# Kernel tuning notes

Measured on AMD Instinct MI355X. Metric: run time of the kernel, lower is better.

The kernel has to match this reference:

```python
import jax, jax.numpy as jnp
import numpy as np

D_MODEL = 1024
HEADS = 16
D_K = D_MODEL // HEADS  # 64
LN_EPS = 1e-5


def setup_inputs() -> dict:
    key = jax.random.key(0)
    ks = jax.random.split(key, 9)
    B, S = 4, 2048
    x = jax.random.normal(ks[0], (B, S, D_MODEL), dtype=jnp.float32)
    s = 1.0 / np.sqrt(D_K)
    # Per-head linear weights, stacked over heads: [H, d_in, d_out]
    Wq = jax.random.uniform(ks[1], (HEADS, D_K, D_K), jnp.float32, -s, s)
    Wk = jax.random.uniform(ks[2], (HEADS, D_K, D_K), jnp.float32, -s, s)
    Wv = jax.random.uniform(ks[3], (HEADS, D_K, D_K), jnp.float32, -s, s)
    bq = jax.random.uniform(ks[4], (HEADS, D_K), jnp.float32, -s, s)
    bk = jax.random.uniform(ks[5], (HEADS, D_K), jnp.float32, -s, s)
    bv = jax.random.uniform(ks[6], (HEADS, D_K), jnp.float32, -s, s)
    gamma = jnp.ones((D_MODEL,), jnp.float32)
    beta = jnp.zeros((D_MODEL,), jnp.float32)
    return {"x": x, "Wq": Wq, "Wk": Wk, "Wv": Wv,
            "bq": bq, "bk": bk, "bv": bv, "gamma": gamma, "beta": beta}


def reference(x, Wq, Wk, Wv, bq, bk, bv, gamma, beta):
    B, S, D = x.shape
    scale = jnp.sqrt(jnp.asarray(D_K, x.dtype))
    # chunk(x, heads, -1) == reshape to [B,S,H,d_k]
    xh = x.reshape(B, S, HEADS, D_K)
    # Batched per-head linears (replaces the Python loop over heads)
    Q = jnp.einsum('bshd,hde->bshe', xh, Wq) + bq  # [B,S,H,d_k]
    K = jnp.einsum('bshd,hde->bshe', xh, Wk) + bk
    V = jnp.einsum('bshd,hde->bshe', xh, Wv) + bv
    scores = jnp.einsum('bshd,bthd->bhst', Q, K) / scale  # [B,H,S,S]
    A = jax.nn.softmax(scores, axis=-1)
    out = jnp.einsum('bhst,bthd->bshd', A, V).reshape(B, S, D)
    # dropout is identity in eval mode; residual + LayerNorm
    y = out + x
    mu = jnp.mean(y, axis=-1, keepdims=True)
    var = jnp.mean((y - mu) ** 2, axis=-1, keepdims=True)
    return (y - mu) * jax.lax.rsqrt(var + LN_EPS) * gamma + beta
```

## Files before the change

kernel.cpp:

```cpp
#include <hip/hip_runtime.h>
#include <math.h>

typedef __bf16 bf16_t;
typedef __bf16 bf16x8 __attribute__((ext_vector_type(8)));
typedef __bf16 bf16x4 __attribute__((ext_vector_type(4)));
typedef short short4v __attribute__((ext_vector_type(4)));
typedef float f32x4 __attribute__((ext_vector_type(4)));

#define LOG2E 1.4426950408889634f

#if __has_builtin(__builtin_amdgcn_exp2f)
#define FAST_EXP2(x) __builtin_amdgcn_exp2f(x)
#else
#define FAST_EXP2(x) exp2f(x)
#endif

constexpr int BATCH = 4;
constexpr int SEQ = 2048;
constexpr int NHEADS = 16;
constexpr int DK = 64;
constexpr int DMODEL = 1024;
constexpr int NTOK = BATCH * SEQ;

constexpr size_t WT_OFF   = 0;
constexpr size_t BIAS_OFF = WT_OFF + (size_t)3*16*64*64*2;
constexpr size_t Q_OFF    = BIAS_OFF + (size_t)3*16*64*4;
constexpr size_t QSZ      = (size_t)BATCH*NHEADS*SEQ*DK*2;
constexpr size_t K_OFF    = Q_OFF + QSZ;
constexpr size_t VT_OFF   = K_OFF + QSZ;
constexpr size_t O_OFF    = VT_OFF + QSZ;

__global__ __launch_bounds__(256) void prep_kernel(
    const float* __restrict__ Wq, const float* __restrict__ Wk,
    const float* __restrict__ Wv, const float* __restrict__ bq,
    const float* __restrict__ bk, const float* __restrict__ bv,
    bf16_t* __restrict__ Wt, float* __restrict__ bias)
{
    const float QS = 0.125f * LOG2E;
    int i = blockIdx.x * 256 + threadIdx.x;
    if (i < 3*16*64*64) {
        int d = i & 63, e = (i >> 6) & 63, h = (i >> 12) & 15, p = i >> 16;
        const float* W = (p == 0) ? Wq : (p == 1) ? Wk : Wv;
        float v = W[(h*64 + d)*64 + e] * ((p == 0) ? QS : 1.0f);
        Wt[i] = (bf16_t)v;
    }
    if (i < 3*16*64) {
        int e = i & 63, h = (i >> 6) & 15, p = i >> 10;
        const float* bb = (p == 0) ? bq : (p == 1) ? bk : bv;
        bias[i] = bb[h*64 + e] * ((p == 0) ? QS : 1.0f);
    }
}

__global__ __launch_bounds__(256) void qkv_kernel(
    const float* __restrict__ x, const bf16_t* __restrict__ Wt,
    const float* __restrict__ bias,
    bf16_t* __restrict__ Q, bf16_t* __restrict__ Kg, bf16_t* __restrict__ Vt)
{
    constexpr int QSTR = 72;
    __shared__ bf16_t Slds[4][16 * QSTR];
    const int tid = threadIdx.x;
    const int w = tid >> 6, lane = tid & 63;
    const int ln = lane & 15, quad = lane >> 4;
    const int gw = blockIdx.x * 4 + w;
    const int h = gw & 15, tt = gw >> 4;
    const int t0 = tt * 16;
    const int b = t0 >> 11;
    const int s0 = t0 & 2047;
    const int bh = b * 16 + h;

    bf16x8 afrag[2];
#pragma unroll
    for (int kc = 0; kc < 2; kc++) {
        const float* xp = &x[(size_t)(t0 + ln)*DMODEL + h*DK + kc*32 + quad*8];
        float4 u0 = *(const float4*)xp;
        float4 u1 = *(const float4*)(xp + 4);
        bf16x8 a;
        a[0]=(bf16_t)u0.x; a[1]=(bf16_t)u0.y; a[2]=(bf16_t)u0.z; a[3]=(bf16_t)u0.w;
        a[4]=(bf16_t)u1.x; a[5]=(bf16_t)u1.y; a[6]=(bf16_t)u1.z; a[7]=(bf16_t)u1.w;
        afrag[kc] = a;
    }

#pragma unroll
    for (int p = 0; p < 3; p++) {
#pragma unroll
        for (int nt = 0; nt < 4; nt++) {
            const bf16_t* wp = &Wt[((size_t)((p*16 + h)*64) + nt*16 + ln)*64 + quad*8];
            bf16x8 b0 = *(const bf16x8*)wp;
            bf16x8 b1 = *(const bf16x8*)(wp + 32);
            f32x4 acc = {0.f, 0.f, 0.f, 0.f};
            acc = __builtin_amdgcn_mfma_f32_16x16x32_bf16(afrag[0], b0, acc, 0, 0, 0);
            acc = __builtin_amdgcn_mfma_f32_16x16x32_bf16(afrag[1], b1, acc, 0, 0, 0);
            float bv = bias[(p*16 + h)*64 + nt*16 + ln];
#pragma unroll
            for (int r = 0; r < 4; r++)
                Slds[w][(quad*4 + r)*QSTR + nt*16 + ln] = (bf16_t)(acc[r] + bv);
        }
        if (p < 2) {
            bf16_t* dst = (p == 0) ? Q : Kg;
            const int row = lane >> 2, c = (lane & 3) * 16;
            bf16_t* dp = &dst[((size_t)bh*SEQ + s0 + row)*DK + c];
            *(uint4*)dp       = *(const uint4*)&Slds[w][row*QSTR + c];
            *(uint4*)(dp + 8) = *(const uint4*)&Slds[w][row*QSTR + c + 8];
        } else {
            unsigned int packed[8];
#pragma unroll
            for (int i = 0; i < 8; i++) {
                unsigned short lo = __builtin_bit_cast(unsigned short, Slds[w][(2*i  )*QSTR + lane]);
                unsigned short hi = __builtin_bit_cast(unsigned short, Slds[w][(2*i+1)*QSTR + lane]);
                packed[i] = (unsigned)lo | ((unsigned)hi << 16);
            }
            bf16_t* vp = &Vt[((size_t)bh*DK + lane)*SEQ + s0];
            uint4 v0; v0.x = packed[0]; v0.y = packed[1]; v0.z = packed[2]; v0.w = packed[3];
            uint4 v1; v1.x = packed[4]; v1.y = packed[5]; v1.z = packed[6]; v1.w = packed[7];
            *(uint4*)(vp)     = v0;
            *(uint4*)(vp + 8) = v1;
        }
    }
}

__global__ __launch_bounds__(256, 2) void flash_kernel(
    const bf16_t* __restrict__ Q, const bf16_t* __restrict__ Kg,
    const bf16_t* __restrict__ Vt, bf16_t* __restrict__ O)
{
    constexpr int LSTR = 72;
    __shared__ union {
        struct { bf16_t K[64 * LSTR]; bf16_t V[64 * LSTR]; } kv;
        bf16_t O[4][32 * LSTR];
    } sh;

    const int tid = threadIdx.x;
    const int w = tid >> 6, lane = tid & 63;
    const int ln = lane & 15, quad = lane >> 4;
    const int bh = blockIdx.x >> 4;
    const int qt = blockIdx.x & 15;
    const int q0 = qt * 128 + w * 32;

    bf16x8 qfrag[2][2];
#pragma unroll
    for (int st = 0; st < 2; st++)
#pragma unroll
        for (int kc = 0; kc < 2; kc++)
            qfrag[st][kc] = *(const bf16x8*)
                &Q[((size_t)bh*SEQ + q0 + st*16 + ln)*DK + kc*32 + quad*8];

    f32x4 o[2][4];
#pragma unroll
    for (int st = 0; st < 2; st++)
#pragma unroll
        for (int dt = 0; dt < 4; dt++)
            o[st][dt] = (f32x4){0.f, 0.f, 0.f, 0.f};
    float l_[2] = {0.f, 0.f};

    const bf16_t* kbase = &Kg[(size_t)bh * SEQ * DK];
    const bf16_t* vbase = &Vt[(size_t)bh * DK * SEQ];

    const int srow = tid >> 3, scol = (tid & 7) * 8;

    for (int ci = 0; ci < SEQ / 64; ci++) {
        __syncthreads();
        {
            uint4 k0 = *(const uint4*)&kbase[((size_t)(ci*64 + srow))*DK + scol];
            uint4 k1 = *(const uint4*)&kbase[((size_t)(ci*64 + srow + 32))*DK + scol];
            uint4 v0 = *(const uint4*)&vbase[(size_t)srow*SEQ + ci*64 + scol];
            uint4 v1 = *(const uint4*)&vbase[(size_t)(srow + 32)*SEQ + ci*64 + scol];
            *(uint4*)&sh.kv.K[srow*LSTR + scol]        = k0;
            *(uint4*)&sh.kv.K[(srow + 32)*LSTR + scol] = k1;
            *(uint4*)&sh.kv.V[srow*LSTR + scol]        = v0;
            *(uint4*)&sh.kv.V[(srow + 32)*LSTR + scol] = v1;
        }
        __syncthreads();

        f32x4 sfrag[2][4];
#pragma unroll
        for (int kt = 0; kt < 4; kt++) {
            bf16x8 ka0 = *(const bf16x8*)&sh.kv.K[(kt*16 + ln)*LSTR + quad*8];
            bf16x8 ka1 = *(const bf16x8*)&sh.kv.K[(kt*16 + ln)*LSTR + 32 + quad*8];
#pragma unroll
            for (int st = 0; st < 2; st++) {
                f32x4 acc = {0.f, 0.f, 0.f, 0.f};
                acc = __builtin_amdgcn_mfma_f32_16x16x32_bf16(ka0, qfrag[st][0], acc, 0, 0, 0);
                acc = __builtin_amdgcn_mfma_f32_16x16x32_bf16(ka1, qfrag[st][1], acc, 0, 0, 0);
                sfrag[st][kt] = acc;
            }
        }

        short4v pfrag[2][4];
#pragma unroll
        for (int st = 0; st < 2; st++) {
            float sum = 0.f;
#pragma unroll
            for (int kt = 0; kt < 4; kt++) {
                bf16x4 pb;
#pragma unroll
                for (int r = 0; r < 4; r++) {
                    float pv = FAST_EXP2(sfrag[st][kt][r]);
                    sum += pv;
                    pb[r] = (bf16_t)pv;
                }
                pfrag[st][kt] = __builtin_bit_cast(short4v, pb);
            }
            l_[st] += sum;
        }

#pragma unroll
        for (int kt = 0; kt < 4; kt++) {
#pragma unroll
            for (int dt = 0; dt < 4; dt++) {
                short4v va = *(const short4v*)
                    &sh.kv.V[(dt*16 + ln)*LSTR + kt*16 + quad*4];
                o[0][dt] = __builtin_amdgcn_mfma_f32_16x16x16bf16_1k(
                    va, pfrag[0][kt], o[0][dt], 0, 0, 0);
                o[1][dt] = __builtin_amdgcn_mfma_f32_16x16x16bf16_1k(
                    va, pfrag[1][kt], o[1][dt], 0, 0, 0);
            }
        }
    }

    __syncthreads();
#pragma unroll
    for (int st = 0; st < 2; st++) {
        float l = l_[st];
        l += __shfl_xor(l, 16);
        l += __shfl_xor(l, 32);
        float rl = 1.0f / l;
#pragma unroll
        for (int dt = 0; dt < 4; dt++)
#pragma unroll
            for (int r = 0; r < 4; r++)
                sh.O[w][(st*16 + ln)*LSTR + dt*16 + quad*4 + r] =
                    (bf16_t)(o[st][dt][r] * rl);
    }
    const int token = lane >> 1, half = lane & 1;
    const int b = bh >> 4, h = bh & 15;
    const size_t s = (size_t)q0 + token;
    bf16_t* op = &O[(((size_t)b*SEQ + s)*NHEADS + h)*DK + half*32];
#pragma unroll
    for (int k2 = 0; k2 < 4; k2++)
        *(uint4*)(op + k2*8) = *(const uint4*)&sh.O[w][token*LSTR + half*32 + k2*8];
}

__global__ __launch_bounds__(256) void ln_kernel(
    const bf16_t* __restrict__ O, const float* __restrict__ x,
    const float* __restrict__ gamma, const float* __restrict__ beta,
    float* __restrict__ out)
{
    const int tid = threadIdx.x;
    const int w = tid >> 6, lane = tid & 63;
    const size_t t = (size_t)blockIdx.x * 4 + w;
    const int d0 = lane * 16;
    const bf16_t* op = &O[t*DMODEL + d0];
    const float* xp = &x[t*DMODEL + d0];

    bf16x8 oa = *(const bf16x8*)op;
    bf16x8 ob = *(const bf16x8*)(op + 8);
    float xs[16];
    ((float4*)xs)[0] = *(const float4*)(xp);
    ((float4*)xs)[1] = *(const float4*)(xp + 4);
    ((float4*)xs)[2] = *(const float4*)(xp + 8);
    ((float4*)xs)[3] = *(const float4*)(xp + 12);

    float yv[16];
    float sum = 0.f, sq = 0.f;
#pragma unroll
    for (int j = 0; j < 16; j++) {
        float ov = (j < 8) ? (float)oa[j] : (float)ob[j - 8];
        yv[j] = ov + xs[j];
        sum += yv[j];
        sq += yv[j] * yv[j];
    }
#pragma unroll
    for (int off = 1; off < 64; off <<= 1) {
        sum += __shfl_xor(sum, off);
        sq  += __shfl_xor(sq, off);
    }
    float mean = sum * (1.0f / DMODEL);
    float var = sq * (1.0f / DMODEL) - mean * mean;
    float rstd = rsqrtf(var + 1e-5f);

    float gs[16], bs[16];
    ((float4*)gs)[0] = *(const float4*)&gamma[d0];
    ((float4*)gs)[1] = *(const float4*)&gamma[d0 + 4];
    ((float4*)gs)[2] = *(const float4*)&gamma[d0 + 8];
    ((float4*)gs)[3] = *(const float4*)&gamma[d0 + 12];
    ((float4*)bs)[0] = *(const float4*)&beta[d0];
    ((float4*)bs)[1] = *(const float4*)&beta[d0 + 4];
    ((float4*)bs)[2] = *(const float4*)&beta[d0 + 8];
    ((float4*)bs)[3] = *(const float4*)&beta[d0 + 12];

    float res[16];
#pragma unroll
    for (int j = 0; j < 16; j++)
        res[j] = (yv[j] - mean) * rstd * gs[j] + bs[j];
    float* outp = &out[t*DMODEL + d0];
    *(float4*)(outp)      = *(float4*)&res[0];
    *(float4*)(outp + 4)  = *(float4*)&res[4];
    *(float4*)(outp + 8)  = *(float4*)&res[8];
    *(float4*)(outp + 12) = *(float4*)&res[12];
}

extern "C" void kernel_launch(void* const* d_in, const int* in_sizes, int n_in,
                              void* d_out, int out_size, void* d_ws, size_t ws_size,
                              hipStream_t stream) {
    const float* x     = (const float*)d_in[0];
    const float* Wq    = (const float*)d_in[1];
    const float* Wk    = (const float*)d_in[2];
    const float* Wv    = (const float*)d_in[3];
    const float* bq    = (const float*)d_in[4];
    const float* bk    = (const float*)d_in[5];
    const float* bv    = (const float*)d_in[6];
    const float* gamma = (const float*)d_in[7];
    const float* beta  = (const float*)d_in[8];

    char* ws = (char*)d_ws;
    bf16_t* Wt   = (bf16_t*)(ws + WT_OFF);
    float*  bias = (float*)(ws + BIAS_OFF);
    bf16_t* Qb   = (bf16_t*)(ws + Q_OFF);
    bf16_t* Kb   = (bf16_t*)(ws + K_OFF);
    bf16_t* Vtb  = (bf16_t*)(ws + VT_OFF);
    bf16_t* Ob   = (bf16_t*)(ws + O_OFF);

    prep_kernel<<<768, 256, 0, stream>>>(Wq, Wk, Wv, bq, bk, bv, Wt, bias);
    qkv_kernel<<<NTOK*NHEADS/16/4, 256, 0, stream>>>(x, Wt, bias, Qb, Kb, Vtb);
    flash_kernel<<<BATCH*NHEADS*(SEQ/128), 256, 0, stream>>>(Qb, Kb, Vtb, Ob);
    ln_kernel<<<NTOK/4, 256, 0, stream>>>(Ob, x, gamma, beta, (float*)d_out);
}
```

Before: 224.9 us.

## Double the flash KV tile to 128 and register-prefetch the next tile

The flash attention loop now processes 128 keys per iteration instead of 64, which halves the number of barrier pairs. The next K/V tile is loaded into registers while the current one is computed, so global-load latency overlaps with MFMA work. The fp32-to-bf16 conversion of P becomes a byte-permute truncation instead of a rounding conversion. In exchange, LDS use and register pressure go up, which may lower occupancy, and truncation changes rounding slightly.

Result: slower. 322.7 us (+43.5%).

```diff
diff --git a/kernel.cpp b/kernel.cpp
--- a/kernel.cpp
+++ b/kernel.cpp
@@ -122,10 +122,11 @@
     const bf16_t* __restrict__ Q, const bf16_t* __restrict__ Kg,
     const bf16_t* __restrict__ Vt, bf16_t* __restrict__ O)
 {
-    constexpr int LSTR = 72;
+    constexpr int KSTR = 72;
+    constexpr int VSTR = 136;
     __shared__ union {
-        struct { bf16_t K[64 * LSTR]; bf16_t V[64 * LSTR]; } kv;
-        bf16_t O[4][32 * LSTR];
+        struct { bf16_t K[128 * KSTR]; bf16_t V[64 * VSTR]; } kv;
+        bf16_t O[4][32 * 72];
     } sh;
 
     const int tid = threadIdx.x;
@@ -154,64 +155,84 @@
     const bf16_t* kbase = &Kg[(size_t)bh * SEQ * DK];
     const bf16_t* vbase = &Vt[(size_t)bh * DK * SEQ];
 
-    const int srow = tid >> 3, scol = (tid & 7) * 8;
-
-    for (int ci = 0; ci < SEQ / 64; ci++) {
+    const int krow = tid >> 3, kcol = (tid & 7) * 8;
+    const int vrow = tid >> 4, vcol = (tid & 15) * 8;
+
+    uint4 kreg[4], vreg[4];
+#pragma unroll
+    for (int r = 0; r < 4; r++) {
+        kreg[r] = *(const uint4*)&kbase[(size_t)(krow + r*32)*DK + kcol];
+        vreg[r] = *(const uint4*)&vbase[(size_t)(vrow + r*16)*SEQ + vcol];
+    }
+
+    for (int ci = 0; ci < SEQ/128; ci++) {
         __syncthreads();
+#pragma unroll
+        for (int r = 0; r < 4; r++) {
+            *(uint4*)&sh.kv.K[(krow + r*32)*KSTR + kcol] = kreg[r];
+            *(uint4*)&sh.kv.V[(vrow + r*16)*VSTR + vcol] = vreg[r];
+        }
         {
-            uint4 k0 = *(const uint4*)&kbase[((size_t)(ci*64 + srow))*DK + scol];
-            uint4 k1 = *(const uint4*)&kbase[((size_t)(ci*64 + srow + 32))*DK + scol];
-            uint4 v0 = *(const uint4*)&vbase[(size_t)srow*SEQ + ci*64 + scol];
-            uint4 v1 = *(const uint4*)&vbase[(size_t)(srow + 32)*SEQ + ci*64 + scol];
-            *(uint4*)&sh.kv.K[srow*LSTR + scol]        = k0;
-            *(uint4*)&sh.kv.K[(srow + 32)*LSTR + scol] = k1;
-            *(uint4*)&sh.kv.V[srow*LSTR + scol]        = v0;
-            *(uint4*)&sh.kv.V[(srow + 32)*LSTR + scol] = v1;
+            const int cn = (ci + 1) & (SEQ/128 - 1);
+#pragma unroll
+            for (int r = 0; r < 4; r++) {
+                kreg[r] = *(const uint4*)&kbase[(size_t)(cn*128 + krow + r*32)*DK + kcol];
+                vreg[r] = *(const uint4*)&vbase[(size_t)(vrow + r*16)*SEQ + cn*128 + vcol];
+            }
         }
         __syncthreads();
 
-        f32x4 sfrag[2][4];
-#pragma unroll
-        for (int kt = 0; kt < 4; kt++) {
-            bf16x8 ka0 = *(const bf16x8*)&sh.kv.K[(kt*16 + ln)*LSTR + quad*8];
-            bf16x8 ka1 = *(const bf16x8*)&sh.kv.K[(kt*16 + ln)*LSTR + 32 + quad*8];
+#pragma unroll
+        for (int hh = 0; hh < 2; hh++) {
+            f32x4 sfrag[2][4];
+#pragma unroll
+            for (int kt = 0; kt < 4; kt++) {
+                const int kr = hh*64 + kt*16 + ln;
+                bf16x8 ka0 = *(const bf16x8*)&sh.kv.K[kr*KSTR + quad*8];
+                bf16x8 ka1 = *(const bf16x8*)&sh.kv.K[kr*KSTR + 32 + quad*8];
+#pragma unroll
+                for (int st = 0; st < 2; st++) {
+                    f32x4 acc = {0.f, 0.f, 0.f, 0.f};
+                    acc = __builtin_amdgcn_mfma_f32_16x16x32_bf16(ka0, qfrag[st][0], acc, 0, 0, 0);
+                    acc = __builtin_amdgcn_mfma_f32_16x16x32_bf16(ka1, qfrag[st][1], acc, 0, 0, 0);
+                    sfrag[st][kt] = acc;
+                }
+            }
+
+            short4v pfrag[2][4];
 #pragma unroll
             for (int st = 0; st < 2; st++) {
-                f32x4 acc = {0.f, 0.f, 0.f, 0.f};
-                acc = __builtin_amdgcn_mfma_f32_16x16x32_bf16(ka0, qfrag[st][0], acc, 0, 0, 0);
-                acc = __builtin_amdgcn_mfma_f32_16x16x32_bf16(ka1, qfrag[st][1], acc, 0, 0, 0);
-                sfrag[st][kt] = acc;
-            }
-        }
-
-        short4v pfrag[2][4];
-#pragma unroll
-        for (int st = 0; st < 2; st++) {
-            float sum = 0.f;
+                float sum = 0.f;
+#pragma unroll
+                for (int kt = 0; kt < 4; kt++) {
+                    float e0 = FAST_EXP2(sfrag[st][kt][0]);
+                    float e1 = FAST_EXP2(sfrag[st][kt][1]);
+                    float e2 = FAST_EXP2(sfrag[st][kt][2]);
+                    float e3 = FAST_EXP2(sfrag[st][kt][3]);
+                    sum += (e0 + e1) + (e2 + e3);
+                    unsigned u0 = __builtin_bit_cast(unsigned, e0);
+                    unsigned u1 = __builtin_bit_cast(unsigned, e1);
+                    unsigned u2 = __builtin_bit_cast(unsigned, e2);
+                    unsigned u3 = __builtin_bit_cast(unsigned, e3);
+                    uint2 pk;
+                    pk.x = __builtin_amdgcn_perm(u1, u0, 0x07060302);
+                    pk.y = __builtin_amdgcn_perm(u3, u2, 0x07060302);
+                    pfrag[st][kt] = __builtin_bit_cast(short4v, pk);
+                }
+                l_[st] += sum;
+            }
+
 #pragma unroll
             for (int kt = 0; kt < 4; kt++) {
-                bf16x4 pb;
-#pragma unroll
-                for (int r = 0; r < 4; r++) {
-                    float pv = FAST_EXP2(sfrag[st][kt][r]);
-                    sum += pv;
-                    pb[r] = (bf16_t)pv;
+#pragma unroll
+                for (int dt = 0; dt < 4; dt++) {
+                    short4v va = *(const short4v*)
+                        &sh.kv.V[(dt*16 + ln)*VSTR + hh*64 + kt*16 + quad*4];
+                    o[0][dt] = __builtin_amdgcn_mfma_f32_16x16x16bf16_1k(
+                        va, pfrag[0][kt], o[0][dt], 0, 0, 0);
+                    o[1][dt] = __builtin_amdgcn_mfma_f32_16x16x16bf16_1k(
+                        va, pfrag[1][kt], o[1][dt], 0, 0, 0);
                 }
-                pfrag[st][kt] = __builtin_bit_cast(short4v, pb);
-            }
-            l_[st] += sum;
-        }
-
-#pragma unroll
-        for (int kt = 0; kt < 4; kt++) {
-#pragma unroll
-            for (int dt = 0; dt < 4; dt++) {
-                short4v va = *(const short4v*)
-                    &sh.kv.V[(dt*16 + ln)*LSTR + kt*16 + quad*4];
-                o[0][dt] = __builtin_amdgcn_mfma_f32_16x16x16bf16_1k(
-                    va, pfrag[0][kt], o[0][dt], 0, 0, 0);
-                o[1][dt] = __builtin_amdgcn_mfma_f32_16x16x16bf16_1k(
-                    va, pfrag[1][kt], o[1][dt], 0, 0, 0);
             }
         }
     }
@@ -227,7 +248,7 @@
         for (int dt = 0; dt < 4; dt++)
 #pragma unroll
             for (int r = 0; r < 4; r++)
-                sh.O[w][(st*16 + ln)*LSTR + dt*16 + quad*4 + r] =
+                sh.O[w][(st*16 + ln)*72 + dt*16 + quad*4 + r] =
                     (bf16_t)(o[st][dt][r] * rl);
     }
     const int token = lane >> 1, half = lane & 1;
@@ -236,7 +257,7 @@
     bf16_t* op = &O[(((size_t)b*SEQ + s)*NHEADS + h)*DK + half*32];
 #pragma unroll
     for (int k2 = 0; k2 < 4; k2++)
-        *(uint4*)(op + k2*8) = *(const uint4*)&sh.O[w][token*LSTR + half*32 + k2*8];
+        *(uint4*)(op + k2*8) = *(const uint4*)&sh.O[w][token*72 + half*32 + k2*8];
 }
 
 __global__ __launch_bounds__(256) void ln_kernel(
```
